# Kernel tuning notes

Hardware: AMD Instinct MI355X
Metric: run time of the kernel (lower is better)

The kernel has to match this reference:

```python
import jax, jax.numpy as jnp
import numpy as np

WIRES = 4
LAYERS = 3
B = 1024
P = 14 * 14  # 196 patches


def setup_inputs() -> dict:
    key = jax.random.key(0)
    k1, k2, k3 = jax.random.split(key, 3)
    x = jax.random.uniform(k1, (B, 1, 28, 28), jnp.float32)
    q_params = jax.random.normal(k2, (LAYERS, WIRES), jnp.float32)
    W = jax.random.normal(k3, (10, 4 * 14 * 14), jnp.float32) * 0.02
    b = jnp.zeros((10,), jnp.float32)
    return {"x": x, "q_params": q_params, "W": W, "b": b}


def _cnot(state, ctrl, tgt):
    # state: [B,P,2,2,2,2]; wire w lives on axis 2+w
    c_ax, t_ax = 2 + ctrl, 2 + tgt
    s0, s1 = jnp.split(state, 2, axis=c_ax)
    s1 = jnp.flip(s1, axis=t_ax)  # flip target when control=1
    return jnp.concatenate([s0, s1], axis=c_ax)


def _circuit(xp, q_params):
    # xp: [B,P,4] RX angles per wire. Returns <Z_w> per wire: [B,P,4].
    Bn, Pn = xp.shape[0], xp.shape[1]
    state = jnp.zeros((Bn, Pn, 2, 2, 2, 2), jnp.complex64).at[:, :, 0, 0, 0, 0].set(1.0)
    for i in range(LAYERS):
        # RX(x[w]) on each wire (angle varies per batch/patch)
        for w in range(WIRES):
            half = xp[:, :, w] * 0.5
            c = jnp.cos(half).astype(jnp.complex64)
            s = (-1j) * jnp.sin(half).astype(jnp.complex64)
            mat = jnp.stack([jnp.stack([c, s], -1), jnp.stack([s, c], -1)], -2)  # [B,P,2,2]
            st = jnp.moveaxis(state, 2 + w, -1)
            st = jnp.einsum('BPij,BPuvwj->BPuvwi', mat, st)
            state = jnp.moveaxis(st, -1, 2 + w)
        state = _cnot(state, 0, 1)
        state = _cnot(state, 2, 3)
        # RZ(params[i,w]) on each wire (scalar phase, diagonal gate)
        for w in range(WIRES):
            phi = q_params[i, w].astype(jnp.complex64)
            ph = jnp.stack([jnp.exp(-0.5j * phi), jnp.exp(0.5j * phi)])  # [2]
            st = jnp.moveaxis(state, 2 + w, -1) * ph
            state = jnp.moveaxis(st, -1, 2 + w)
    probs = state.real ** 2 + state.imag ** 2  # [B,P,2,2,2,2]
    zs = []
    for w in range(WIRES):
        axes = tuple(a for a in range(2, 6) if a != 2 + w)
        m = probs.sum(axes)  # [B,P,2]
        zs.append(m[..., 0] - m[..., 1])
    return jnp.stack(zs, -1)  # [B,P,4]


def reference(x, q_params, W, b):
    Bn = x.shape[0]
    # 2x2 patches in row-major (r,c) order; per-patch flatten order matches
    # view of x[:,0,r:r+2,c:c+2]: [tl, tr, bl, br]
    xp = x[:, 0].reshape(Bn, 14, 2, 14, 2).transpose(0, 1, 3, 2, 4).reshape(Bn, P, 4)
    z = _circuit(xp, q_params)            # [B,196,4]
    feats = z.reshape(Bn, P * 4).astype(jnp.float32)  # cat order: patch-major, wire-minor
    logits = feats @ W.T + b
    return jax.nn.log_softmax(logits, axis=-1)
```

## Files before the change

kernel.cpp:

```cpp
#include <hip/hip_runtime.h>
#include <math.h>

#define LAYERS  3
#define PATCHES 196


__device__ __forceinline__ void pair_layer(
    float r[4], float im[4],
    float cu, float su, float cv, float sv,
    float cS, float sS, float cD, float sD)
{
    {
        float t0r=r[0], t0i=im[0], t1r=r[2], t1i=im[2];
        r[0]=fmaf(cu,t0r, su*t1i); im[0]=fmaf(cu,t0i,-su*t1r);
        r[2]=fmaf(cu,t1r, su*t0i); im[2]=fmaf(cu,t1i,-su*t0r);
    }
    {
        float t0r=r[1], t0i=im[1], t1r=r[3], t1i=im[3];
        r[1]=fmaf(cu,t0r, su*t1i); im[1]=fmaf(cu,t0i,-su*t1r);
        r[3]=fmaf(cu,t1r, su*t0i); im[3]=fmaf(cu,t1i,-su*t0r);
    }
    {
        float t0r=r[0], t0i=im[0], t1r=r[1], t1i=im[1];
        r[0]=fmaf(cv,t0r, sv*t1i); im[0]=fmaf(cv,t0i,-sv*t1r);
        r[1]=fmaf(cv,t1r, sv*t0i); im[1]=fmaf(cv,t1i,-sv*t0r);
    }
    {
        float t0r=r[2], t0i=im[2], t1r=r[3], t1i=im[3];
        r[2]=fmaf(cv,t0r, sv*t1i); im[2]=fmaf(cv,t0i,-sv*t1r);
        r[3]=fmaf(cv,t1r, sv*t0i); im[3]=fmaf(cv,t1i,-sv*t0r);
    }
    { float tr=r[2]; r[2]=r[3]; r[3]=tr; float ti=im[2]; im[2]=im[3]; im[3]=ti; }
    {
        float rr, ii;
        rr=r[0]; ii=im[0];  r[0]=fmaf(rr,cS,  ii*sS); im[0]=fmaf(ii,cS, -rr*sS);
        rr=r[1]; ii=im[1];  r[1]=fmaf(rr,cD,  ii*sD); im[1]=fmaf(ii,cD, -rr*sD);
        rr=r[2]; ii=im[2];  r[2]=fmaf(rr,cD, -ii*sD); im[2]=fmaf(ii,cD,  rr*sD);
        rr=r[3]; ii=im[3];  r[3]=fmaf(rr,cS, -ii*sS); im[3]=fmaf(ii,cS,  rr*sS);
    }
}

__global__ __launch_bounds__(256) void quanv_fused(
    const float* __restrict__ x,
    const float* __restrict__ qp,
    const float* __restrict__ Wt,
    const float* __restrict__ bias,
    float* __restrict__ out)
{
    __shared__ float wsum[4][10];
    __shared__ float lg[10];

    const int b = blockIdx.x;
    const int t = threadIdx.x;

    float cS[LAYERS][2], sS[LAYERS][2], cD[LAYERS][2], sD[LAYERS][2];
    #pragma unroll
    for (int l = 0; l < LAYERS; ++l) {
        #pragma unroll
        for (int p = 0; p < 2; ++p) {
            const float pu = qp[l*4 + 2*p], pv = qp[l*4 + 2*p + 1];
            __sincosf(0.5f*(pu+pv), &sS[l][p], &cS[l][p]);
            __sincosf(0.5f*(pu-pv), &sD[l][p], &cD[l][p]);
        }
    }

    float z[4] = {0.f, 0.f, 0.f, 0.f};
    if (t < PATCHES) {
        const int r = t / 14, cc = t % 14;
        const float* xb = x + (size_t)b * 784;
        const float2 top = *reinterpret_cast<const float2*>(xb + (2*r)*28 + 2*cc);
        const float2 bot = *reinterpret_cast<const float2*>(xb + (2*r+1)*28 + 2*cc);
        float cw[4], sw[4];
        __sincosf(0.5f * top.x, &sw[0], &cw[0]);
        __sincosf(0.5f * top.y, &sw[1], &cw[1]);
        __sincosf(0.5f * bot.x, &sw[2], &cw[2]);
        __sincosf(0.5f * bot.y, &sw[3], &cw[3]);

        float Ar[4], Ai[4], Br[4], Bi[4];
        {
            const float m0=cw[0]*cw[1], m1=cw[0]*sw[1], m2=sw[0]*cw[1], m3=sw[0]*sw[1];
            const float cs=cS[0][0], ss=sS[0][0], cd=cD[0][0], sd=sD[0][0];
            Ar[0]= m0*cs;  Ai[0]=-m0*ss;
            Ar[1]=-m1*sd;  Ai[1]=-m1*cd;
            Ar[3]= m2*ss;  Ai[3]=-m2*cs;
            Ar[2]=-m3*cd;  Ai[2]=-m3*sd;
        }
        {
            const float m0=cw[2]*cw[3], m1=cw[2]*sw[3], m2=sw[2]*cw[3], m3=sw[2]*sw[3];
            const float cs=cS[0][1], ss=sS[0][1], cd=cD[0][1], sd=sD[0][1];
            Br[0]= m0*cs;  Bi[0]=-m0*ss;
            Br[1]=-m1*sd;  Bi[1]=-m1*cd;
            Br[3]= m2*ss;  Bi[3]=-m2*cs;
            Br[2]=-m3*cd;  Bi[2]=-m3*sd;
        }

        #pragma unroll
        for (int l = 1; l < LAYERS; ++l) {
            pair_layer(Ar, Ai, cw[0],sw[0], cw[1],sw[1],
                       cS[l][0],sS[l][0], cD[l][0],sD[l][0]);
            pair_layer(Br, Bi, cw[2],sw[2], cw[3],sw[3],
                       cS[l][1],sS[l][1], cD[l][1],sD[l][1]);
        }

        {
            const float p0=fmaf(Ar[0],Ar[0],Ai[0]*Ai[0]);
            const float p1=fmaf(Ar[1],Ar[1],Ai[1]*Ai[1]);
            const float p2=fmaf(Ar[2],Ar[2],Ai[2]*Ai[2]);
            const float p3=fmaf(Ar[3],Ar[3],Ai[3]*Ai[3]);
            z[0] = (p0+p1) - (p2+p3);
            z[1] = (p0+p2) - (p1+p3);
        }
        {
            const float p0=fmaf(Br[0],Br[0],Bi[0]*Bi[0]);
            const float p1=fmaf(Br[1],Br[1],Bi[1]*Bi[1]);
            const float p2=fmaf(Br[2],Br[2],Bi[2]*Bi[2]);
            const float p3=fmaf(Br[3],Br[3],Bi[3]*Bi[3]);
            z[2] = (p0+p1) - (p2+p3);
            z[3] = (p0+p2) - (p1+p3);
        }
    }

    float part[10];
    if (t < PATCHES) {
        const float4* W4 = reinterpret_cast<const float4*>(Wt);
        #pragma unroll
        for (int k = 0; k < 10; ++k) {
            const float4 w = W4[k * 196 + t];
            part[k] = fmaf(z[0], w.x, fmaf(z[1], w.y, fmaf(z[2], w.z, z[3] * w.w)));
        }
    } else {
        #pragma unroll
        for (int k = 0; k < 10; ++k) part[k] = 0.f;
    }
    #pragma unroll
    for (int k = 0; k < 10; ++k) {
        #pragma unroll
        for (int off = 32; off > 0; off >>= 1)
            part[k] += __shfl_down(part[k], off, 64);
    }
    const int wave = t >> 6, lane = t & 63;
    if (lane == 0) {
        #pragma unroll
        for (int k = 0; k < 10; ++k) wsum[wave][k] = part[k];
    }
    __syncthreads();
    if (t < 10)
        lg[t] = bias[t] + wsum[0][t] + wsum[1][t] + wsum[2][t] + wsum[3][t];
    __syncthreads();
    if (t < 10) {
        float mx = lg[0];
        #pragma unroll
        for (int k = 1; k < 10; ++k) mx = fmaxf(mx, lg[k]);
        float se = 0.f;
        #pragma unroll
        for (int k = 0; k < 10; ++k) se += expf(lg[k] - mx);
        out[b * 10 + t] = lg[t] - (mx + logf(se));
    }
}

extern "C" void kernel_launch(void* const* d_in, const int* in_sizes, int n_in,
                              void* d_out, int out_size, void* d_ws, size_t ws_size,
                              hipStream_t stream) {
    const float* x    = (const float*)d_in[0];
    const float* qp   = (const float*)d_in[1];
    const float* W    = (const float*)d_in[2];
    const float* bias = (const float*)d_in[3];
    float* out = (float*)d_out;

    const int B = in_sizes[0] / 784;
    quanv_fused<<<B, 256, 0, stream>>>(x, qp, W, bias, out);
}
```

Measured before the change: 64.36 us.

## Split logit reduction across lane pairs and share phase constants via LDS

Phase-gate sincos values are now computed once per block by 12 spare threads and stored in shared memory, so each thread no longer runs 12 sincos calls. Adjacent lanes exchange their z values, and each lane computes 5 of the 10 logits over two patches. This halves the number of shuffle-reduction chains and keeps the same W loads. The final log-softmax uses a 16-lane shuffle reduction instead of a second barrier plus serial loops. In exchange it adds an extra __syncthreads before the circuit and LDS reads of the phase values inside the inner loop.

```diff
diff --git a/kernel.cpp b/kernel.cpp
--- a/kernel.cpp
+++ b/kernel.cpp
@@ -47,39 +47,40 @@
     const float* __restrict__ bias,
     float* __restrict__ out)
 {
+    __shared__ float2 ph[LAYERS * 4];
     __shared__ float wsum[4][10];
-    __shared__ float lg[10];
 
     const int b = blockIdx.x;
     const int t = threadIdx.x;
 
-    float cS[LAYERS][2], sS[LAYERS][2], cD[LAYERS][2], sD[LAYERS][2];
-    #pragma unroll
-    for (int l = 0; l < LAYERS; ++l) {
-        #pragma unroll
-        for (int p = 0; p < 2; ++p) {
-            const float pu = qp[l*4 + 2*p], pv = qp[l*4 + 2*p + 1];
-            __sincosf(0.5f*(pu+pv), &sS[l][p], &cS[l][p]);
-            __sincosf(0.5f*(pu-pv), &sD[l][p], &cD[l][p]);
-        }
+    if (t >= 208 && t < 208 + LAYERS * 4) {
+        const int j = t - 208;
+        const int l = j >> 2, p = (j >> 1) & 1, d = j & 1;
+        const float pu = qp[l*4 + 2*p], pv = qp[l*4 + 2*p + 1];
+        float s, c;
+        __sincosf(0.5f * (d ? (pu - pv) : (pu + pv)), &s, &c);
+        ph[j] = make_float2(c, s);
     }
 
-    float z[4] = {0.f, 0.f, 0.f, 0.f};
+    float cw[4], sw[4];
     if (t < PATCHES) {
         const int r = t / 14, cc = t % 14;
         const float* xb = x + (size_t)b * 784;
         const float2 top = *reinterpret_cast<const float2*>(xb + (2*r)*28 + 2*cc);
         const float2 bot = *reinterpret_cast<const float2*>(xb + (2*r+1)*28 + 2*cc);
-        float cw[4], sw[4];
         __sincosf(0.5f * top.x, &sw[0], &cw[0]);
         __sincosf(0.5f * top.y, &sw[1], &cw[1]);
         __sincosf(0.5f * bot.x, &sw[2], &cw[2]);
         __sincosf(0.5f * bot.y, &sw[3], &cw[3]);
+    }
+    __syncthreads();
 
+    float z[4] = {0.f, 0.f, 0.f, 0.f};
+    if (t < PATCHES) {
         float Ar[4], Ai[4], Br[4], Bi[4];
         {
             const float m0=cw[0]*cw[1], m1=cw[0]*sw[1], m2=sw[0]*cw[1], m3=sw[0]*sw[1];
-            const float cs=cS[0][0], ss=sS[0][0], cd=cD[0][0], sd=sD[0][0];
+            const float cs=ph[0].x, ss=ph[0].y, cd=ph[1].x, sd=ph[1].y;
             Ar[0]= m0*cs;  Ai[0]=-m0*ss;
             Ar[1]=-m1*sd;  Ai[1]=-m1*cd;
             Ar[3]= m2*ss;  Ai[3]=-m2*cs;
@@ -87,7 +88,7 @@
         }
         {
             const float m0=cw[2]*cw[3], m1=cw[2]*sw[3], m2=sw[2]*cw[3], m3=sw[2]*sw[3];
-            const float cs=cS[0][1], ss=sS[0][1], cd=cD[0][1], sd=sD[0][1];
+            const float cs=ph[2].x, ss=ph[2].y, cd=ph[3].x, sd=ph[3].y;
             Br[0]= m0*cs;  Bi[0]=-m0*ss;
             Br[1]=-m1*sd;  Bi[1]=-m1*cd;
             Br[3]= m2*ss;  Bi[3]=-m2*cs;
@@ -97,9 +98,9 @@
         #pragma unroll
         for (int l = 1; l < LAYERS; ++l) {
             pair_layer(Ar, Ai, cw[0],sw[0], cw[1],sw[1],
-                       cS[l][0],sS[l][0], cD[l][0],sD[l][0]);
+                       ph[l*4+0].x, ph[l*4+0].y, ph[l*4+1].x, ph[l*4+1].y);
             pair_layer(Br, Bi, cw[2],sw[2], cw[3],sw[3],
-                       cS[l][1],sS[l][1], cD[l][1],sD[l][1]);
+                       ph[l*4+2].x, ph[l*4+2].y, ph[l*4+3].x, ph[l*4+3].y);
         }
 
         {
@@ -120,41 +121,57 @@
         }
     }
 
-    float part[10];
+    float oz[4];
+    #pragma unroll
+    for (int j = 0; j < 4; ++j) oz[j] = __shfl_xor(z[j], 1, 64);
+
+    float part[5];
     if (t < PATCHES) {
+        const int p0 = t & ~1;
+        const int kbase = (t & 1) * 5;
+        const float* zp0 = (t & 1) ? oz : z;
+        const float* zp1 = (t & 1) ? z : oz;
         const float4* W4 = reinterpret_cast<const float4*>(Wt);
         #pragma unroll
-        for (int k = 0; k < 10; ++k) {
-            const float4 w = W4[k * 196 + t];
-            part[k] = fmaf(z[0], w.x, fmaf(z[1], w.y, fmaf(z[2], w.z, z[3] * w.w)));
+        for (int k = 0; k < 5; ++k) {
+            const float4 w0 = W4[(kbase + k) * 196 + p0];
+            const float4 w1 = W4[(kbase + k) * 196 + p0 + 1];
+            float acc;
+            acc = fmaf(zp0[0], w0.x, fmaf(zp0[1], w0.y, fmaf(zp0[2], w0.z, zp0[3] * w0.w)));
+            acc = fmaf(zp1[0], w1.x, fmaf(zp1[1], w1.y, fmaf(zp1[2], w1.z, fmaf(zp1[3], w1.w, acc))));
+            part[k] = acc;
         }
     } else {
         #pragma unroll
-        for (int k = 0; k < 10; ++k) part[k] = 0.f;
+        for (int k = 0; k < 5; ++k) part[k] = 0.f;
     }
     #pragma unroll
-    for (int k = 0; k < 10; ++k) {
+    for (int k = 0; k < 5; ++k) {
         #pragma unroll
-        for (int off = 32; off > 0; off >>= 1)
-            part[k] += __shfl_down(part[k], off, 64);
+        for (int off = 2; off <= 32; off <<= 1)
+            part[k] += __shfl_xor(part[k], off, 64);
     }
     const int wave = t >> 6, lane = t & 63;
-    if (lane == 0) {
+    if (lane < 2) {
         #pragma unroll
-        for (int k = 0; k < 10; ++k) wsum[wave][k] = part[k];
+        for (int k = 0; k < 5; ++k) wsum[wave][lane * 5 + k] = part[k];
     }
     __syncthreads();
-    if (t < 10)
-        lg[t] = bias[t] + wsum[0][t] + wsum[1][t] + wsum[2][t] + wsum[3][t];
-    __syncthreads();
-    if (t < 10) {
-        float mx = lg[0];
+
+    if (t < 16) {
+        const float v = (t < 10)
+            ? (bias[t] + wsum[0][t] + wsum[1][t] + wsum[2][t] + wsum[3][t])
+            : -1e30f;
+        float mx = v;
         #pragma unroll
-        for (int k = 1; k < 10; ++k) mx = fmaxf(mx, lg[k]);
-        float se = 0.f;
+        for (int off = 8; off > 0; off >>= 1)
+            mx = fmaxf(mx, __shfl_xor(mx, off, 16));
+        float se = (t < 10) ? expf(v - mx) : 0.f;
         #pragma unroll
-        for (int k = 0; k < 10; ++k) se += expf(lg[k] - mx);
-        out[b * 10 + t] = lg[t] - (mx + logf(se));
+        for (int off = 8; off > 0; off >>= 1)
+            se += __shfl_xor(se, off, 16);
+        if (t < 10)
+            out[b * 10 + t] = v - (mx + logf(se));
     }
 }
 
```

After: 62.70 us. 2.6% less time.
